# Optimization experiments

Hardware: AMD Instinct MI355X
Metric: run time of the kernel (lower is better)

## Reference

```python
import jax, jax.numpy as jnp
import numpy as np

N = 100000
E = 1600000
F_IN, H, C = 128, 128, 64


def setup_inputs() -> dict:
    key = jax.random.key(0)
    ks = jax.random.split(key, 8)
    x = jax.random.normal(ks[0], (N, F_IN), dtype=jnp.float32)
    edge_index = jax.random.randint(ks[1], (2, E), 0, N, dtype=jnp.int64)
    s = lambda fi: (1.0 / np.sqrt(fi))
    # SAGEConv1: lin_l (applied to mean-aggregated neighbors, has bias), lin_r (root, no bias)
    W1l = jax.random.uniform(ks[2], (H, F_IN), jnp.float32, -s(F_IN), s(F_IN))
    b1 = jnp.zeros((H,), jnp.float32)
    W1r = jax.random.uniform(ks[3], (H, F_IN), jnp.float32, -s(F_IN), s(F_IN))
    # SAGEConv2
    W2l = jax.random.uniform(ks[4], (C, H), jnp.float32, -s(H), s(H))
    b2 = jnp.zeros((C,), jnp.float32)
    W2r = jax.random.uniform(ks[5], (C, H), jnp.float32, -s(H), s(H))
    return {"x": x, "edge_index": edge_index, "W1l": W1l, "b1": b1, "W1r": W1r,
            "W2l": W2l, "b2": b2, "W2r": W2r}


def _mean_aggr(x, src, dst):
    # mean over incoming neighbors (PyG flow: edge_index[0]=source -> edge_index[1]=target)
    msg = x[src]                                            # [E, F] big gather
    summed = jax.ops.segment_sum(msg, dst, num_segments=N)  # [N, F]
    cnt = jax.ops.segment_sum(jnp.ones((src.shape[0],), x.dtype), dst, num_segments=N)
    return summed / jnp.clip(cnt, 1.0)[:, None]


def _sage_conv(x, src, dst, Wl, b, Wr):
    agg = _mean_aggr(x, src, dst)
    return agg @ Wl.T + b + x @ Wr.T


def _iconv(x, src, dst):
    # weight-free GCN propagation: D^-1/2 (A + I) D^-1/2 @ x
    loops = jnp.arange(N, dtype=src.dtype)
    s2 = jnp.concatenate([src, loops])
    d2 = jnp.concatenate([dst, loops])
    deg = jax.ops.segment_sum(jnp.ones((s2.shape[0],), x.dtype), d2, num_segments=N)
    dis = jnp.where(deg > 0, jax.lax.rsqrt(jnp.maximum(deg, 1.0)), 0.0)
    norm = dis[s2] * dis[d2]                               # [E+N]
    return jax.ops.segment_sum(norm[:, None] * x[s2], d2, num_segments=N)


def reference(x, edge_index, W1l, b1, W1r, W2l, b2, W2r):
    src, dst = edge_index[0], edge_index[1]
    h = jax.nn.relu(_sage_conv(x, src, dst, W1l, b1, W1r))
    # F.dropout(training=False) -> identity in eval mode
    h = _sage_conv(h, src, dst, W2l, b2, W2r)
    return _iconv(h, src, dst)
```

## Files before the change

kernel.cpp:

```cpp
#include <hip/hip_runtime.h>

#define GN 100000
#define GE 1600000
#define GF 128
#define GH 128
#define GC 64

#define NB 392
#define SLABSZ 5376
#define P1_EDGES 4096
#define P1_BLOCKS ((GE + P1_EDGES - 1) / P1_EDGES)
#define CASTX_BLOCKS 12500

typedef __attribute__((ext_vector_type(8))) short v8s;
typedef __attribute__((ext_vector_type(4))) float v4f;
typedef __attribute__((ext_vector_type(2))) float v2f;

__device__ __forceinline__ unsigned short f2bf(float f) {
    union { float f; unsigned u; } a; a.f = f;
    unsigned r = a.u + 0x7fff + ((a.u >> 16) & 1);
    return (unsigned short)(r >> 16);
}
__device__ __forceinline__ float bf2f(unsigned short b) {
    union { unsigned u; float f; } a; a.u = ((unsigned)b) << 16;
    return a.f;
}
__device__ __forceinline__ v2f cvt2(unsigned w) {
    union { unsigned u; float f; } lo, hi;
    lo.u = w << 16; hi.u = w & 0xffff0000u;
    return (v2f){lo.f, hi.f};
}

__device__ __forceinline__ int block_excl_scan256(int v, volatile int* ws, int tid) {
    int lane = tid & 63, w = tid >> 6;
    int s = v;
    #pragma unroll
    for (int off = 1; off < 64; off <<= 1) {
        int t = __shfl_up(s, off);
        if (lane >= off) s += t;
    }
    if (lane == 63) ws[w] = s;
    __syncthreads();
    int wbase = 0;
    if (w > 0) wbase += ws[0];
    if (w > 1) wbase += ws[1];
    if (w > 2) wbase += ws[2];
    __syncthreads();
    return wbase + s - v;
}

__global__ __launch_bounds__(256) void prep_kernel(
    unsigned* __restrict__ slab, int* __restrict__ bucket_cnt,
    const int* __restrict__ src, const int* __restrict__ dst,
    unsigned short* __restrict__ xb, const float* __restrict__ x,
    unsigned short* w1l, unsigned short* w1r,
    unsigned short* w2l, unsigned short* w2r,
    const float* W1l, const float* W1r,
    const float* W2l, const float* W2r)
{
    __shared__ int hist[512];
    __shared__ int scanex[512];
    __shared__ int cursor[512];
    __shared__ int gbase[512];
    __shared__ int wsS[4];
    __shared__ unsigned stage[P1_EDGES];
    __shared__ unsigned short sbid[P1_EDGES];

    int tid = threadIdx.x;
    int blk = blockIdx.x;

    if (blk >= P1_BLOCKS) {
        int cb = blk - P1_BLOCKS;
        if (cb < CASTX_BLOCKS) {
            int i = cb * 256 + tid;
            float4 v = ((const float4*)x)[i];
            ushort4 u;
            u.x = f2bf(v.x); u.y = f2bf(v.y); u.z = f2bf(v.z); u.w = f2bf(v.w);
            ((ushort4*)xb)[i] = u;
            return;
        }
        int i = (cb - CASTX_BLOCKS) * 256 + tid;
        const float* s; unsigned short* d; int off;
        if      (i <  4096) { s = W1l; d = w1l; off = i; }
        else if (i <  8192) { s = W1r; d = w1r; off = i - 4096; }
        else if (i < 10240) { s = W2l; d = w2l; off = i - 8192; }
        else if (i < 12288) { s = W2r; d = w2r; off = i - 10240; }
        else return;
        float4 v = ((const float4*)s)[off];
        ushort4 u;
        u.x = f2bf(v.x); u.y = f2bf(v.y); u.z = f2bf(v.z); u.w = f2bf(v.w);
        ((ushort4*)d)[off] = u;
        return;
    }

    int e0 = blk * P1_EDGES;
    int nE = min(P1_EDGES, GE - e0);

    unsigned pk[16]; int bk[16];
    hist[tid] = 0; hist[tid + 256] = 0;
    __syncthreads();
    #pragma unroll
    for (int j = 0; j < 16; ++j) {
        int i = j * 256 + tid;
        if (i < nE) {
            int e = e0 + i;
            int d = dst[e], s = src[e];
            int b = d >> 8;
            pk[j] = ((unsigned)(d & 255) << 17) | (unsigned)s;
            bk[j] = b;
            atomicAdd(&hist[b], 1);
        } else bk[j] = -1;
    }
    __syncthreads();
    int a0 = hist[2 * tid], a1 = hist[2 * tid + 1];
    int pbase = block_excl_scan256(a0 + a1, wsS, tid);
    scanex[2 * tid] = pbase;          cursor[2 * tid] = pbase;
    scanex[2 * tid + 1] = pbase + a0; cursor[2 * tid + 1] = pbase + a0;
    __syncthreads();
    #pragma unroll
    for (int j = 0; j < 16; ++j) {
        if (bk[j] >= 0) {
            int pos = atomicAdd(&cursor[bk[j]], 1);
            stage[pos] = pk[j];
            sbid[pos] = (unsigned short)bk[j];
        }
    }
    for (int b = tid; b < NB; b += 256) {
        int c = hist[b];
        gbase[b] = c ? atomicAdd(&bucket_cnt[b], c) : 0;
    }
    __syncthreads();
    for (int i = tid; i < nE; i += 256) {
        int b = sbid[i];
        int go = gbase[b] + (i - scanex[b]);
        if (go < SLABSZ)
            slab[(size_t)b * SLABSZ + go] = stage[i];
    }
}

__global__ __launch_bounds__(256) void bucket_pass2_kernel(
    int* __restrict__ csr, int* __restrict__ row_ptr,
    float* __restrict__ invc, float* __restrict__ dis,
    const unsigned* __restrict__ slab, const int* __restrict__ bucket_cnt)
{
    __shared__ int deg_l[256];
    __shared__ int cur[256];
    __shared__ int wsS[4];
    __shared__ int bstart_s;
    __shared__ unsigned stage[SLABSZ];

    int t = threadIdx.x;
    int b = blockIdx.x;

    int c0 = (2 * t < NB) ? bucket_cnt[2 * t] : 0;
    int c1 = (2 * t + 1 < NB) ? bucket_cnt[2 * t + 1] : 0;
    int pb = block_excl_scan256(c0 + c1, wsS, t);
    if (2 * t == b)     bstart_s = pb;
    if (2 * t + 1 == b) bstart_s = pb + c0;
    if (b == NB - 1 && t == 0) row_ptr[GN] = GE;

    int cnt = min(bucket_cnt[b], SLABSZ);
    const unsigned* sp = slab + (size_t)b * SLABSZ;
    deg_l[t] = 0;
    __syncthreads();
    int base = bstart_s;
    for (int i = t; i < cnt; i += 256)
        atomicAdd(&deg_l[sp[i] >> 17], 1);
    __syncthreads();
    int dg = deg_l[t];
    int ex = block_excl_scan256(dg, wsS, t);
    cur[t] = ex;
    __syncthreads();
    int d = b * 256 + t;
    if (d < GN) {
        row_ptr[d] = base + ex;
        float c = (float)dg;
        invc[d] = 1.0f / fmaxf(c, 1.0f);
        dis[d] = rsqrtf(c + 1.0f);
    }
    for (int i = t; i < cnt; i += 256) {
        unsigned p = sp[i];
        int pos = atomicAdd(&cur[p >> 17], 1);
        stage[pos] = p & 0x1FFFFu;
    }
    __syncthreads();
    for (int i = t; i < cnt; i += 256)
        csr[base + i] = (int)stage[i];
}

__global__ __launch_bounds__(64, 2) void fused_gemm_kernel(
    unsigned short* __restrict__ P, unsigned short* __restrict__ Q,
    const unsigned short* __restrict__ A1, const unsigned short* __restrict__ A2,
    const unsigned short* __restrict__ W1, const unsigned short* __restrict__ W2,
    const unsigned short* __restrict__ Wl, const unsigned short* __restrict__ Wr,
    const float* __restrict__ b1, const float* __restrict__ b2, int M)
{
    __shared__ unsigned short hs[64][136];

    int lane = threadIdx.x;
    int lm = lane & 15, quad = lane >> 4;
    int m_base = blockIdx.x * 64;

    v4f acc[4][8];
    #pragma unroll
    for (int mt = 0; mt < 4; ++mt)
        #pragma unroll
        for (int nt = 0; nt < 8; ++nt) acc[mt][nt] = (v4f){0.f,0.f,0.f,0.f};

    #pragma unroll
    for (int ks = 0; ks < 4; ++ks) {
        int koff = ks * 32 + quad * 8;
        v8s a1[4], a2[4];
        #pragma unroll
        for (int mt = 0; mt < 4; ++mt) {
            int row = m_base + mt * 16 + lm;
            if (row < M) {
                a1[mt] = *(const v8s*)(A1 + (size_t)row * 128 + koff);
                a2[mt] = *(const v8s*)(A2 + (size_t)row * 128 + koff);
            } else {
                a1[mt] = (v8s){0,0,0,0,0,0,0,0};
                a2[mt] = (v8s){0,0,0,0,0,0,0,0};
            }
        }
        v8s w1[8], w2[8];
        #pragma unroll
        for (int nt = 0; nt < 8; ++nt) {
            int col = nt * 16 + lm;
            w1[nt] = *(const v8s*)(W1 + (size_t)col * 128 + koff);
            w2[nt] = *(const v8s*)(W2 + (size_t)col * 128 + koff);
        }
        #pragma unroll
        for (int mt = 0; mt < 4; ++mt)
            #pragma unroll
            for (int nt = 0; nt < 8; ++nt) {
                acc[mt][nt] = __builtin_amdgcn_mfma_f32_16x16x32_bf16(a1[mt], w1[nt], acc[mt][nt], 0, 0, 0);
                acc[mt][nt] = __builtin_amdgcn_mfma_f32_16x16x32_bf16(a2[mt], w2[nt], acc[mt][nt], 0, 0, 0);
            }
    }

    #pragma unroll
    for (int mt = 0; mt < 4; ++mt)
        #pragma unroll
        for (int r = 0; r < 4; ++r) {
            int rl = mt * 16 + quad * 4 + r;
            #pragma unroll
            for (int nt = 0; nt < 8; ++nt) {
                int col = nt * 16 + lm;
                float v = acc[mt][nt][r] + b1[col];
                hs[rl][col] = f2bf(fmaxf(v, 0.f));
            }
        }

    v4f accP[4][4], accQ[4][4];
    #pragma unroll
    for (int mt = 0; mt < 4; ++mt)
        #pragma unroll
        for (int nt = 0; nt < 4; ++nt) {
            accP[mt][nt] = (v4f){0.f,0.f,0.f,0.f};
            accQ[mt][nt] = (v4f){0.f,0.f,0.f,0.f};
        }

    #pragma unroll
    for (int ks = 0; ks < 4; ++ks) {
        int koff = ks * 32 + quad * 8;
        v8s af[4], bl[4], br[4];
        #pragma unroll
        for (int mt = 0; mt < 4; ++mt)
            af[mt] = *(const v8s*)&hs[mt * 16 + lm][koff];
        #pragma unroll
        for (int nt = 0; nt < 4; ++nt) {
            int col = nt * 16 + lm;
            bl[nt] = *(const v8s*)(Wl + (size_t)col * 128 + koff);
            br[nt] = *(const v8s*)(Wr + (size_t)col * 128 + koff);
        }
        #pragma unroll
        for (int mt = 0; mt < 4; ++mt)
            #pragma unroll
            for (int nt = 0; nt < 4; ++nt) {
                accP[mt][nt] = __builtin_amdgcn_mfma_f32_16x16x32_bf16(af[mt], bl[nt], accP[mt][nt], 0, 0, 0);
                accQ[mt][nt] = __builtin_amdgcn_mfma_f32_16x16x32_bf16(af[mt], br[nt], accQ[mt][nt], 0, 0, 0);
            }
    }

    #pragma unroll
    for (int mt = 0; mt < 4; ++mt)
        #pragma unroll
        for (int r = 0; r < 4; ++r) {
            int row = m_base + mt * 16 + quad * 4 + r;
            if (row >= M) continue;
            #pragma unroll
            for (int nt = 0; nt < 4; ++nt) {
                int col = nt * 16 + lm;
                P[(size_t)row * 64 + col] = f2bf(accP[mt][nt][r]);
                Q[(size_t)row * 64 + col] = f2bf(accQ[mt][nt][r] + b2[col]);
            }
        }
}

__global__ __launch_bounds__(256) void gather_mean128_kernel(
    unsigned short* __restrict__ out, const unsigned short* __restrict__ in,
    const float* __restrict__ invc, const int* __restrict__ row_ptr,
    const int* __restrict__ csr, int N)
{
    int wid = (blockIdx.x * 256 + threadIdx.x) >> 6;
    int lane = threadIdx.x & 63;
    if (wid >= N) return;
    int beg = __builtin_amdgcn_readfirstlane(row_ptr[wid]);
    int end = __builtin_amdgcn_readfirstlane(row_ptr[wid + 1]);
    int d = end - beg;
    int grp = lane >> 4, lx = lane & 15;
    v2f a0 = {0.f,0.f}, a1 = {0.f,0.f}, a2 = {0.f,0.f}, a3 = {0.f,0.f};

    int nf = d >> 2;
    #pragma unroll 4
    for (int t = 0; t < nf; ++t) {
        int j = beg + t * 4;
        int s0 = csr[j], s1 = csr[j + 1], s2 = csr[j + 2], s3 = csr[j + 3];
        int sa = (lane & 16) ? s1 : s0;
        int sb = (lane & 16) ? s3 : s2;
        int ss = (lane & 32) ? sb : sa;
        uint4 v = ((const uint4*)(in + (size_t)ss * 128))[lx];
        a0 += cvt2(v.x); a1 += cvt2(v.y); a2 += cvt2(v.z); a3 += cvt2(v.w);
    }
    int rem = d & 3;
    if (rem) {
        int j = beg + nf * 4;
        int c1 = (rem > 1) ? 1 : 0;
        int c2 = (rem > 2) ? 2 : c1;
        int s0 = csr[j], s1 = csr[j + c1], s2 = csr[j + c2], s3 = s2;
        int sa = (lane & 16) ? s1 : s0;
        int sb = (lane & 16) ? s3 : s2;
        int ss = (lane & 32) ? sb : sa;
        uint4 v = ((const uint4*)(in + (size_t)ss * 128))[lx];
        bool ok = grp < rem;
        v.x = ok ? v.x : 0u; v.y = ok ? v.y : 0u;
        v.z = ok ? v.z : 0u; v.w = ok ? v.w : 0u;
        a0 += cvt2(v.x); a1 += cvt2(v.y); a2 += cvt2(v.z); a3 += cvt2(v.w);
    }
    a0.x += __shfl_xor(a0.x, 16); a0.y += __shfl_xor(a0.y, 16);
    a1.x += __shfl_xor(a1.x, 16); a1.y += __shfl_xor(a1.y, 16);
    a2.x += __shfl_xor(a2.x, 16); a2.y += __shfl_xor(a2.y, 16);
    a3.x += __shfl_xor(a3.x, 16); a3.y += __shfl_xor(a3.y, 16);
    a0.x += __shfl_xor(a0.x, 32); a0.y += __shfl_xor(a0.y, 32);
    a1.x += __shfl_xor(a1.x, 32); a1.y += __shfl_xor(a1.y, 32);
    a2.x += __shfl_xor(a2.x, 32); a2.y += __shfl_xor(a2.y, 32);
    a3.x += __shfl_xor(a3.x, 32); a3.y += __shfl_xor(a3.y, 32);
    if (grp == 0) {
        float ic = invc[wid];
        uint4 o;
        o.x = (unsigned)f2bf(a0.x * ic) | ((unsigned)f2bf(a0.y * ic) << 16);
        o.y = (unsigned)f2bf(a1.x * ic) | ((unsigned)f2bf(a1.y * ic) << 16);
        o.z = (unsigned)f2bf(a2.x * ic) | ((unsigned)f2bf(a2.y * ic) << 16);
        o.w = (unsigned)f2bf(a3.x * ic) | ((unsigned)f2bf(a3.y * ic) << 16);
        ((uint4*)(out + (size_t)wid * 128))[lx] = o;
    }
}

__global__ __launch_bounds__(256) void gather_combine_kernel(
    unsigned short* __restrict__ h2s, const unsigned short* __restrict__ p,
    const unsigned short* __restrict__ q,
    const float* __restrict__ invc, const float* __restrict__ dis,
    const int* __restrict__ row_ptr, const int* __restrict__ csr, int N)
{
    int wid = (blockIdx.x * 256 + threadIdx.x) >> 6;
    int lane = threadIdx.x & 63;
    if (wid >= N) return;
    int beg = __builtin_amdgcn_readfirstlane(row_ptr[wid]);
    int end = __builtin_amdgcn_readfirstlane(row_ptr[wid + 1]);
    int d = end - beg;
    int grp = lane >> 3, lx = lane & 7;
    v2f a0 = {0.f,0.f}, a1 = {0.f,0.f}, a2 = {0.f,0.f}, a3 = {0.f,0.f};

    int nf = d >> 3;
    #pragma unroll 2
    for (int t = 0; t < nf; ++t) {
        int j = beg + t * 8;
        int s0 = csr[j],     s1 = csr[j + 1], s2 = csr[j + 2], s3 = csr[j + 3];
        int s4 = csr[j + 4], s5 = csr[j + 5], s6 = csr[j + 6], s7 = csr[j + 7];
        int t0 = (lane & 8) ? s1 : s0; int t1 = (lane & 8) ? s3 : s2;
        int t2 = (lane & 8) ? s5 : s4; int t3 = (lane & 8) ? s7 : s6;
        int u0 = (lane & 16) ? t1 : t0; int u1 = (lane & 16) ? t3 : t2;
        int ss = (lane & 32) ? u1 : u0;
        uint4 v = ((const uint4*)(p + (size_t)ss * 64))[lx];
        a0 += cvt2(v.x); a1 += cvt2(v.y); a2 += cvt2(v.z); a3 += cvt2(v.w);
    }
    int rem = d & 7;
    if (rem) {
        int j = beg + nf * 8;
        int rc = rem - 1;
        int s0 = csr[j];
        int s1 = csr[j + min(1, rc)]; int s2 = csr[j + min(2, rc)];
        int s3 = csr[j + min(3, rc)]; int s4 = csr[j + min(4, rc)];
        int s5 = csr[j + min(5, rc)]; int s6 = csr[j + min(6, rc)];
        int s7 = csr[j + min(7, rc)];
        int t0 = (lane & 8) ? s1 : s0; int t1 = (lane & 8) ? s3 : s2;
        int t2 = (lane & 8) ? s5 : s4; int t3 = (lane & 8) ? s7 : s6;
        int u0 = (lane & 16) ? t1 : t0; int u1 = (lane & 16) ? t3 : t2;
        int ss = (lane & 32) ? u1 : u0;
        uint4 v = ((const uint4*)(p + (size_t)ss * 64))[lx];
        bool ok = grp < rem;
        v.x = ok ? v.x : 0u; v.y = ok ? v.y : 0u;
        v.z = ok ? v.z : 0u; v.w = ok ? v.w : 0u;
        a0 += cvt2(v.x); a1 += cvt2(v.y); a2 += cvt2(v.z); a3 += cvt2(v.w);
    }
    #pragma unroll
    for (int m = 8; m <= 32; m <<= 1) {
        a0.x += __shfl_xor(a0.x, m); a0.y += __shfl_xor(a0.y, m);
        a1.x += __shfl_xor(a1.x, m); a1.y += __shfl_xor(a1.y, m);
        a2.x += __shfl_xor(a2.x, m); a2.y += __shfl_xor(a2.y, m);
        a3.x += __shfl_xor(a3.x, m); a3.y += __shfl_xor(a3.y, m);
    }
    if (grp == 0) {
        float ic = invc[wid], dd = dis[wid];
        uint4 qv = ((const uint4*)(q + (size_t)wid * 64))[lx];
        v2f q0 = cvt2(qv.x), q1 = cvt2(qv.y), q2 = cvt2(qv.z), q3 = cvt2(qv.w);
        uint4 o;
        o.x = (unsigned)f2bf(dd * (a0.x * ic + q0.x)) | ((unsigned)f2bf(dd * (a0.y * ic + q0.y)) << 16);
        o.y = (unsigned)f2bf(dd * (a1.x * ic + q1.x)) | ((unsigned)f2bf(dd * (a1.y * ic + q1.y)) << 16);
        o.z = (unsigned)f2bf(dd * (a2.x * ic + q2.x)) | ((unsigned)f2bf(dd * (a2.y * ic + q2.y)) << 16);
        o.w = (unsigned)f2bf(dd * (a3.x * ic + q3.x)) | ((unsigned)f2bf(dd * (a3.y * ic + q3.y)) << 16);
        ((uint4*)(h2s + (size_t)wid * 64))[lx] = o;
    }
}

__global__ __launch_bounds__(256) void iconv_kernel(
    float* __restrict__ out, const unsigned short* __restrict__ h2s,
    const float* __restrict__ dis, const int* __restrict__ row_ptr,
    const int* __restrict__ csr, int N)
{
    int wid = (blockIdx.x * 256 + threadIdx.x) >> 6;
    int lane = threadIdx.x & 63;
    if (wid >= N) return;
    int beg = __builtin_amdgcn_readfirstlane(row_ptr[wid]);
    int end = __builtin_amdgcn_readfirstlane(row_ptr[wid + 1]);
    int d = end - beg;
    int grp = lane >> 3, lx = lane & 7;
    v2f a0 = {0.f,0.f}, a1 = {0.f,0.f}, a2 = {0.f,0.f}, a3 = {0.f,0.f};

    int nf = d >> 3;
    #pragma unroll 2
    for (int t = 0; t < nf; ++t) {
        int j = beg + t * 8;
        int s0 = csr[j],     s1 = csr[j + 1], s2 = csr[j + 2], s3 = csr[j + 3];
        int s4 = csr[j + 4], s5 = csr[j + 5], s6 = csr[j + 6], s7 = csr[j + 7];
        int t0 = (lane & 8) ? s1 : s0; int t1 = (lane & 8) ? s3 : s2;
        int t2 = (lane & 8) ? s5 : s4; int t3 = (lane & 8) ? s7 : s6;
        int u0 = (lane & 16) ? t1 : t0; int u1 = (lane & 16) ? t3 : t2;
        int ss = (lane & 32) ? u1 : u0;
        uint4 v = ((const uint4*)(h2s + (size_t)ss * 64))[lx];
        a0 += cvt2(v.x); a1 += cvt2(v.y); a2 += cvt2(v.z); a3 += cvt2(v.w);
    }
    int rem = d & 7;
    if (rem) {
        int j = beg + nf * 8;
        int rc = rem - 1;
        int s0 = csr[j];
        int s1 = csr[j + min(1, rc)]; int s2 = csr[j + min(2, rc)];
        int s3 = csr[j + min(3, rc)]; int s4 = csr[j + min(4, rc)];
        int s5 = csr[j + min(5, rc)]; int s6 = csr[j + min(6, rc)];
        int s7 = csr[j + min(7, rc)];
        int t0 = (lane & 8) ? s1 : s0; int t1 = (lane & 8) ? s3 : s2;
        int t2 = (lane & 8) ? s5 : s4; int t3 = (lane & 8) ? s7 : s6;
        int u0 = (lane & 16) ? t1 : t0; int u1 = (lane & 16) ? t3 : t2;
        int ss = (lane & 32) ? u1 : u0;
        uint4 v = ((const uint4*)(h2s + (size_t)ss * 64))[lx];
        bool ok = grp < rem;
        v.x = ok ? v.x : 0u; v.y = ok ? v.y : 0u;
        v.z = ok ? v.z : 0u; v.w = ok ? v.w : 0u;
        a0 += cvt2(v.x); a1 += cvt2(v.y); a2 += cvt2(v.z); a3 += cvt2(v.w);
    }
    #pragma unroll
    for (int m = 8; m <= 32; m <<= 1) {
        a0.x += __shfl_xor(a0.x, m); a0.y += __shfl_xor(a0.y, m);
        a1.x += __shfl_xor(a1.x, m); a1.y += __shfl_xor(a1.y, m);
        a2.x += __shfl_xor(a2.x, m); a2.y += __shfl_xor(a2.y, m);
        a3.x += __shfl_xor(a3.x, m); a3.y += __shfl_xor(a3.y, m);
    }
    if (grp == 0) {
        uint4 sv = ((const uint4*)(h2s + (size_t)wid * 64))[lx];
        v2f s0 = cvt2(sv.x), s1 = cvt2(sv.y), s2 = cvt2(sv.z), s3 = cvt2(sv.w);
        float dd = dis[wid];
        float4 o0 = make_float4(dd * (a0.x + s0.x), dd * (a0.y + s0.y),
                                dd * (a1.x + s1.x), dd * (a1.y + s1.y));
        float4 o1 = make_float4(dd * (a2.x + s2.x), dd * (a2.y + s2.y),
                                dd * (a3.x + s3.x), dd * (a3.y + s3.y));
        ((float4*)(out + (size_t)wid * 64))[lx * 2]     = o0;
        ((float4*)(out + (size_t)wid * 64))[lx * 2 + 1] = o1;
    }
}

extern "C" void kernel_launch(void* const* d_in, const int* in_sizes, int n_in,
                              void* d_out, int out_size, void* d_ws, size_t ws_size,
                              hipStream_t stream) {
    const float* x   = (const float*)d_in[0];
    const int*   ei  = (const int*)d_in[1];
    const float* W1l = (const float*)d_in[2];
    const float* b1  = (const float*)d_in[3];
    const float* W1r = (const float*)d_in[4];
    const float* W2l = (const float*)d_in[5];
    const float* b2  = (const float*)d_in[6];
    const float* W2r = (const float*)d_in[7];
    float* out = (float*)d_out;

    const int* src = ei;
    const int* dst = ei + GE;

    float* invc = (float*)d_ws;
    float* dis  = invc + GN;
    unsigned short* regA = (unsigned short*)(dis + GN);
    unsigned short* regB = regA + (size_t)GN * 128;
    unsigned short* xb    = regA;
    unsigned short* aggx  = regB;
    unsigned short* w1lb = regB + (size_t)GN * 128;
    unsigned short* w1rb = w1lb + GH * GF;
    unsigned short* w2lb = w1rb + GH * GF;
    unsigned short* w2rb = w2lb + GC * GH;
    int* row_ptr      = (int*)(w2rb + GC * GH);
    int* bucket_cnt   = row_ptr + GN + 1;
    unsigned* slab    = (unsigned*)(bucket_cnt + NB);
    int* csr          = (int*)(slab + (size_t)NB * SLABSZ);
    unsigned short* pq = (unsigned short*)(csr + GE);
    unsigned short* pb = pq;
    unsigned short* qb = pq + (size_t)GN * 64;
    unsigned short* h2s = regB;

    const int T = 256;
    const int g_wave = (GN * 64 + T - 1) / T;
    dim3 g_fused((GN + 63) / 64, 1);

    hipMemsetAsync(bucket_cnt, 0, NB * sizeof(int), stream);
    prep_kernel<<<P1_BLOCKS + CASTX_BLOCKS + 48, T, 0, stream>>>(
        slab, bucket_cnt, src, dst,
        xb, x, w1lb, w1rb, w2lb, w2rb, W1l, W1r, W2l, W2r);

    bucket_pass2_kernel<<<NB, T, 0, stream>>>(csr, row_ptr, invc, dis,
                                              slab, bucket_cnt);

    gather_mean128_kernel<<<g_wave, T, 0, stream>>>(aggx, xb, invc, row_ptr, csr, GN);

    fused_gemm_kernel<<<g_fused, 64, 0, stream>>>(pb, qb, aggx, xb,
                                                  w1lb, w1rb, w2lb, w2rb,
                                                  b1, b2, GN);

    gather_combine_kernel<<<g_wave, T, 0, stream>>>(h2s, pb, qb, invc, dis,
                                                    row_ptr, csr, GN);

    iconv_kernel<<<g_wave, T, 0, stream>>>(out, h2s, dis, row_ptr, csr, GN);
}
```

Measured before the change: 334.4 us.

## Halve GEMM tile height and split gather/GEMM launches into halves

Shrinks the fused GEMM block tile from 64 to 32 rows, loads weight fragments inside the MFMA loop instead of holding them all in registers, and raises the launch-bounds occupancy hint from 2 to 3. It also splits the gather and GEMM kernels into two launches covering half the rows each. The aim is to lower register pressure and raise occupancy in the GEMM. In exchange each weight fragment is reused across fewer rows, and the extra launches add overhead. The launches run back to back on one stream, so the split by itself gives no overlap.

```diff
diff --git a/kernel.cpp b/kernel.cpp
--- a/kernel.cpp
+++ b/kernel.cpp
@@ -188,31 +188,32 @@
         csr[base + i] = (int)stage[i];
 }
 
-__global__ __launch_bounds__(64, 2) void fused_gemm_kernel(
+__global__ __launch_bounds__(64, 3) void fused_gemm_kernel(
     unsigned short* __restrict__ P, unsigned short* __restrict__ Q,
     const unsigned short* __restrict__ A1, const unsigned short* __restrict__ A2,
     const unsigned short* __restrict__ W1, const unsigned short* __restrict__ W2,
     const unsigned short* __restrict__ Wl, const unsigned short* __restrict__ Wr,
-    const float* __restrict__ b1, const float* __restrict__ b2, int M)
+    const float* __restrict__ b1, const float* __restrict__ b2,
+    int m_off, int M)
 {
-    __shared__ unsigned short hs[64][136];
+    __shared__ unsigned short hs[32][136];
 
     int lane = threadIdx.x;
     int lm = lane & 15, quad = lane >> 4;
-    int m_base = blockIdx.x * 64;
-
-    v4f acc[4][8];
-    #pragma unroll
-    for (int mt = 0; mt < 4; ++mt)
+    int m_base = m_off + blockIdx.x * 32;
+
+    v4f acc[2][8];
+    #pragma unroll
+    for (int mt = 0; mt < 2; ++mt)
         #pragma unroll
         for (int nt = 0; nt < 8; ++nt) acc[mt][nt] = (v4f){0.f,0.f,0.f,0.f};
 
     #pragma unroll
     for (int ks = 0; ks < 4; ++ks) {
         int koff = ks * 32 + quad * 8;
-        v8s a1[4], a2[4];
-        #pragma unroll
-        for (int mt = 0; mt < 4; ++mt) {
+        v8s a1[2], a2[2];
+        #pragma unroll
+        for (int mt = 0; mt < 2; ++mt) {
             int row = m_base + mt * 16 + lm;
             if (row < M) {
                 a1[mt] = *(const v8s*)(A1 + (size_t)row * 128 + koff);
@@ -222,24 +223,21 @@
                 a2[mt] = (v8s){0,0,0,0,0,0,0,0};
             }
         }
-        v8s w1[8], w2[8];
         #pragma unroll
         for (int nt = 0; nt < 8; ++nt) {
             int col = nt * 16 + lm;
-            w1[nt] = *(const v8s*)(W1 + (size_t)col * 128 + koff);
-            w2[nt] = *(const v8s*)(W2 + (size_t)col * 128 + koff);
-        }
-        #pragma unroll
-        for (int mt = 0; mt < 4; ++mt)
+            v8s w1 = *(const v8s*)(W1 + (size_t)col * 128 + koff);
+            v8s w2 = *(const v8s*)(W2 + (size_t)col * 128 + koff);
             #pragma unroll
-            for (int nt = 0; nt < 8; ++nt) {
-                acc[mt][nt] = __builtin_amdgcn_mfma_f32_16x16x32_bf16(a1[mt], w1[nt], acc[mt][nt], 0, 0, 0);
-                acc[mt][nt] = __builtin_amdgcn_mfma_f32_16x16x32_bf16(a2[mt], w2[nt], acc[mt][nt], 0, 0, 0);
+            for (int mt = 0; mt < 2; ++mt) {
+                acc[mt][nt] = __builtin_amdgcn_mfma_f32_16x16x32_bf16(a1[mt], w1, acc[mt][nt], 0, 0, 0);
+                acc[mt][nt] = __builtin_amdgcn_mfma_f32_16x16x32_bf16(a2[mt], w2, acc[mt][nt], 0, 0, 0);
             }
-    }
-
-    #pragma unroll
-    for (int mt = 0; mt < 4; ++mt)
+        }
+    }
+
+    #pragma unroll
+    for (int mt = 0; mt < 2; ++mt)
         #pragma unroll
         for (int r = 0; r < 4; ++r) {
             int rl = mt * 16 + quad * 4 + r;
@@ -251,9 +249,9 @@
             }
         }
 
-    v4f accP[4][4], accQ[4][4];
-    #pragma unroll
-    for (int mt = 0; mt < 4; ++mt)
+    v4f accP[2][4], accQ[2][4];
+    #pragma unroll
+    for (int mt = 0; mt < 2; ++mt)
         #pragma unroll
         for (int nt = 0; nt < 4; ++nt) {
             accP[mt][nt] = (v4f){0.f,0.f,0.f,0.f};
@@ -263,27 +261,25 @@
     #pragma unroll
     for (int ks = 0; ks < 4; ++ks) {
         int koff = ks * 32 + quad * 8;
-        v8s af[4], bl[4], br[4];
-        #pragma unroll
-        for (int mt = 0; mt < 4; ++mt)
+        v8s af[2];
+        #pragma unroll
+        for (int mt = 0; mt < 2; ++mt)
             af[mt] = *(const v8s*)&hs[mt * 16 + lm][koff];
         #pragma unroll
         for (int nt = 0; nt < 4; ++nt) {
             int col = nt * 16 + lm;
-            bl[nt] = *(const v8s*)(Wl + (size_t)col * 128 + koff);
-            br[nt] = *(const v8s*)(Wr + (size_t)col * 128 + koff);
-        }
-        #pragma unroll
-        for (int mt = 0; mt < 4; ++mt)
+            v8s bl = *(const v8s*)(Wl + (size_t)col * 128 + koff);
+            v8s br = *(const v8s*)(Wr + (size_t)col * 128 + koff);
             #pragma unroll
-            for (int nt = 0; nt < 4; ++nt) {
-                accP[mt][nt] = __builtin_amdgcn_mfma_f32_16x16x32_bf16(af[mt], bl[nt], accP[mt][nt], 0, 0, 0);
-                accQ[mt][nt] = __builtin_amdgcn_mfma_f32_16x16x32_bf16(af[mt], br[nt], accQ[mt][nt], 0, 0, 0);
+            for (int mt = 0; mt < 2; ++mt) {
+                accP[mt][nt] = __builtin_amdgcn_mfma_f32_16x16x32_bf16(af[mt], bl, accP[mt][nt], 0, 0, 0);
+                accQ[mt][nt] = __builtin_amdgcn_mfma_f32_16x16x32_bf16(af[mt], br, accQ[mt][nt], 0, 0, 0);
             }
-    }
-
-    #pragma unroll
-    for (int mt = 0; mt < 4; ++mt)
+        }
+    }
+
+    #pragma unroll
+    for (int mt = 0; mt < 2; ++mt)
         #pragma unroll
         for (int r = 0; r < 4; ++r) {
             int row = m_base + mt * 16 + quad * 4 + r;
@@ -300,11 +296,11 @@
 __global__ __launch_bounds__(256) void gather_mean128_kernel(
     unsigned short* __restrict__ out, const unsigned short* __restrict__ in,
     const float* __restrict__ invc, const int* __restrict__ row_ptr,
-    const int* __restrict__ csr, int N)
+    const int* __restrict__ csr, int row0, int row1)
 {
-    int wid = (blockIdx.x * 256 + threadIdx.x) >> 6;
+    int wid = row0 + ((blockIdx.x * 256 + threadIdx.x) >> 6);
     int lane = threadIdx.x & 63;
-    if (wid >= N) return;
+    if (wid >= row1) return;
     int beg = __builtin_amdgcn_readfirstlane(row_ptr[wid]);
     int end = __builtin_amdgcn_readfirstlane(row_ptr[wid + 1]);
     int d = end - beg;
@@ -360,11 +356,12 @@
     unsigned short* __restrict__ h2s, const unsigned short* __restrict__ p,
     const unsigned short* __restrict__ q,
     const float* __restrict__ invc, const float* __restrict__ dis,
-    const int* __restrict__ row_ptr, const int* __restrict__ csr, int N)
+    const int* __restrict__ row_ptr, const int* __restrict__ csr,
+    int row0, int row1)
 {
-    int wid = (blockIdx.x * 256 + threadIdx.x) >> 6;
+    int wid = row0 + ((blockIdx.x * 256 + threadIdx.x) >> 6);
     int lane = threadIdx.x & 63;
-    if (wid >= N) return;
+    if (wid >= row1) return;
     int beg = __builtin_amdgcn_readfirstlane(row_ptr[wid]);
     int end = __builtin_amdgcn_readfirstlane(row_ptr[wid + 1]);
     int d = end - beg;
@@ -526,7 +523,7 @@
 
     const int T = 256;
     const int g_wave = (GN * 64 + T - 1) / T;
-    dim3 g_fused((GN + 63) / 64, 1);
+    const int g_half = (50000 * 64) / T;
 
     hipMemsetAsync(bucket_cnt, 0, NB * sizeof(int), stream);
     prep_kernel<<<P1_BLOCKS + CASTX_BLOCKS + 48, T, 0, stream>>>(
@@ -536,14 +533,22 @@
     bucket_pass2_kernel<<<NB, T, 0, stream>>>(csr, row_ptr, invc, dis,
                                               slab, bucket_cnt);
 
-    gather_mean128_kernel<<<g_wave, T, 0, stream>>>(aggx, xb, invc, row_ptr, csr, GN);
-
-    fused_gemm_kernel<<<g_fused, 64, 0, stream>>>(pb, qb, aggx, xb,
-                                                  w1lb, w1rb, w2lb, w2rb,
-                                                  b1, b2, GN);
-
-    gather_combine_kernel<<<g_wave, T, 0, stream>>>(h2s, pb, qb, invc, dis,
-                                                    row_ptr, csr, GN);
+    gather_mean128_kernel<<<g_half, T, 0, stream>>>(aggx, xb, invc, row_ptr, csr,
+                                                    0, 50000);
+    gather_mean128_kernel<<<g_half, T, 0, stream>>>(aggx, xb, invc, row_ptr, csr,
+                                                    50000, GN);
+
+    fused_gemm_kernel<<<1563, 64, 0, stream>>>(pb, qb, aggx, xb,
+                                               w1lb, w1rb, w2lb, w2rb,
+                                               b1, b2, 0, GN);
+    fused_gemm_kernel<<<1562, 64, 0, stream>>>(pb, qb, aggx, xb,
+                                               w1lb, w1rb, w2lb, w2rb,
+                                               b1, b2, 50016, GN);
+
+    gather_combine_kernel<<<g_half, T, 0, stream>>>(h2s, pb, qb, invc, dis,
+                                                    row_ptr, csr, 0, 50000);
+    gather_combine_kernel<<<g_half, T, 0, stream>>>(h2s, pb, qb, invc, dis,
+                                                    row_ptr, csr, 50000, GN);
 
     iconv_kernel<<<g_wave, T, 0, stream>>>(out, h2s, dis, row_ptr, csr, GN);
 }
```

Result: slower. 360.7 us (+7.9%).

## Fuse first-layer mean aggregation into the SAGE GEMM kernel via LDS

Applied to the files above, without the earlier changes.

Merges the 128-wide neighbor mean gather and the two-layer fused GEMM into one kernel. Each 1024-thread block handles 16 nodes: 16 waves each gather one node's neighbors into LDS, then 8 waves compute the first layer with MFMA, and finally the P/Q projections. This removes the aggx write and re-read through global memory and one kernel launch. In exchange the weight reuse per block drops from 64 to 16 rows, weights are reloaded much more often, and half the waves sit idle during the GEMM phases.

```diff
diff --git a/kernel.cpp b/kernel.cpp
--- a/kernel.cpp
+++ b/kernel.cpp
@@ -188,171 +188,118 @@
         csr[base + i] = (int)stage[i];
 }
 
-__global__ __launch_bounds__(64, 2) void fused_gemm_kernel(
+__global__ __launch_bounds__(1024, 8) void sage16_kernel(
     unsigned short* __restrict__ P, unsigned short* __restrict__ Q,
-    const unsigned short* __restrict__ A1, const unsigned short* __restrict__ A2,
+    const unsigned short* __restrict__ xb,
     const unsigned short* __restrict__ W1, const unsigned short* __restrict__ W2,
     const unsigned short* __restrict__ Wl, const unsigned short* __restrict__ Wr,
-    const float* __restrict__ b1, const float* __restrict__ b2, int M)
+    const float* __restrict__ b1, const float* __restrict__ b2,
+    const float* __restrict__ invc, const int* __restrict__ row_ptr,
+    const int* __restrict__ csr)
 {
-    __shared__ unsigned short hs[64][136];
-
-    int lane = threadIdx.x;
+    __shared__ unsigned short hsA[16][136];
+    __shared__ unsigned short hsB[16][136];
+
+    int tid = threadIdx.x;
+    int wv = tid >> 6, lane = tid & 63;
     int lm = lane & 15, quad = lane >> 4;
-    int m_base = blockIdx.x * 64;
-
-    v4f acc[4][8];
-    #pragma unroll
-    for (int mt = 0; mt < 4; ++mt)
+    int m_base = blockIdx.x * 16;
+
+    {
+        int wid = m_base + wv;
+        int beg = __builtin_amdgcn_readfirstlane(row_ptr[wid]);
+        int end = __builtin_amdgcn_readfirstlane(row_ptr[wid + 1]);
+        int d = end - beg;
+        v2f a0 = {0.f,0.f}, a1 = {0.f,0.f}, a2 = {0.f,0.f}, a3 = {0.f,0.f};
+
+        int nf = d >> 2;
+        #pragma unroll 4
+        for (int t = 0; t < nf; ++t) {
+            int j = beg + t * 4;
+            int s0 = csr[j], s1 = csr[j + 1], s2 = csr[j + 2], s3 = csr[j + 3];
+            int sa = (lane & 16) ? s1 : s0;
+            int sb = (lane & 16) ? s3 : s2;
+            int ss = (lane & 32) ? sb : sa;
+            uint4 v = ((const uint4*)(xb + (size_t)ss * 128))[lm];
+            a0 += cvt2(v.x); a1 += cvt2(v.y); a2 += cvt2(v.z); a3 += cvt2(v.w);
+        }
+        int rem = d & 3;
+        if (rem) {
+            int j = beg + nf * 4;
+            int c1 = (rem > 1) ? 1 : 0;
+            int c2 = (rem > 2) ? 2 : c1;
+            int s0 = csr[j], s1 = csr[j + c1], s2 = csr[j + c2], s3 = s2;
+            int sa = (lane & 16) ? s1 : s0;
+            int sb = (lane & 16) ? s3 : s2;
+            int ss = (lane & 32) ? sb : sa;
+            uint4 v = ((const uint4*)(xb + (size_t)ss * 128))[lm];
+            bool ok = quad < rem;
+            v.x = ok ? v.x : 0u; v.y = ok ? v.y : 0u;
+            v.z = ok ? v.z : 0u; v.w = ok ? v.w : 0u;
+            a0 += cvt2(v.x); a1 += cvt2(v.y); a2 += cvt2(v.z); a3 += cvt2(v.w);
+        }
+        a0.x += __shfl_xor(a0.x, 16); a0.y += __shfl_xor(a0.y, 16);
+        a1.x += __shfl_xor(a1.x, 16); a1.y += __shfl_xor(a1.y, 16);
+        a2.x += __shfl_xor(a2.x, 16); a2.y += __shfl_xor(a2.y, 16);
+        a3.x += __shfl_xor(a3.x, 16); a3.y += __shfl_xor(a3.y, 16);
+        a0.x += __shfl_xor(a0.x, 32); a0.y += __shfl_xor(a0.y, 32);
+        a1.x += __shfl_xor(a1.x, 32); a1.y += __shfl_xor(a1.y, 32);
+        a2.x += __shfl_xor(a2.x, 32); a2.y += __shfl_xor(a2.y, 32);
+        a3.x += __shfl_xor(a3.x, 32); a3.y += __shfl_xor(a3.y, 32);
+        if (quad == 0) {
+            float ic = invc[wid];
+            uint4 o;
+            o.x = (unsigned)f2bf(a0.x * ic) | ((unsigned)f2bf(a0.y * ic) << 16);
+            o.y = (unsigned)f2bf(a1.x * ic) | ((unsigned)f2bf(a1.y * ic) << 16);
+            o.z = (unsigned)f2bf(a2.x * ic) | ((unsigned)f2bf(a2.y * ic) << 16);
+            o.w = (unsigned)f2bf(a3.x * ic) | ((unsigned)f2bf(a3.y * ic) << 16);
+            *(uint4*)&hsA[wv][lm * 8] = o;
+        }
+    }
+    __syncthreads();
+
+    if (wv < 8) {
+        int col = wv * 16 + lm;
+        v4f acc = (v4f){0.f,0.f,0.f,0.f};
         #pragma unroll
-        for (int nt = 0; nt < 8; ++nt) acc[mt][nt] = (v4f){0.f,0.f,0.f,0.f};
-
-    #pragma unroll
-    for (int ks = 0; ks < 4; ++ks) {
-        int koff = ks * 32 + quad * 8;
-        v8s a1[4], a2[4];
+        for (int ks = 0; ks < 4; ++ks) {
+            int koff = ks * 32 + quad * 8;
+            v8s a1f = *(const v8s*)&hsA[lm][koff];
+            v8s w1 = *(const v8s*)(W1 + (size_t)col * 128 + koff);
+            acc = __builtin_amdgcn_mfma_f32_16x16x32_bf16(a1f, w1, acc, 0, 0, 0);
+            v8s a2f = *(const v8s*)(xb + (size_t)(m_base + lm) * 128 + koff);
+            v8s w2 = *(const v8s*)(W2 + (size_t)col * 128 + koff);
+            acc = __builtin_amdgcn_mfma_f32_16x16x32_bf16(a2f, w2, acc, 0, 0, 0);
+        }
+        float bv = b1[col];
         #pragma unroll
-        for (int mt = 0; mt < 4; ++mt) {
-            int row = m_base + mt * 16 + lm;
-            if (row < M) {
-                a1[mt] = *(const v8s*)(A1 + (size_t)row * 128 + koff);
-                a2[mt] = *(const v8s*)(A2 + (size_t)row * 128 + koff);
-            } else {
-                a1[mt] = (v8s){0,0,0,0,0,0,0,0};
-                a2[mt] = (v8s){0,0,0,0,0,0,0,0};
-            }
-        }
-        v8s w1[8], w2[8];
+        for (int r = 0; r < 4; ++r)
+            hsB[quad * 4 + r][col] = f2bf(fmaxf(acc[r] + bv, 0.f));
+    }
+    __syncthreads();
+
+    if (wv < 8) {
+        int isQ = wv >> 2;
+        int col = (wv & 3) * 16 + lm;
+        const unsigned short* W = isQ ? Wr : Wl;
+        v4f acc = (v4f){0.f,0.f,0.f,0.f};
         #pragma unroll
-        for (int nt = 0; nt < 8; ++nt) {
-            int col = nt * 16 + lm;
-            w1[nt] = *(const v8s*)(W1 + (size_t)col * 128 + koff);
-            w2[nt] = *(const v8s*)(W2 + (size_t)col * 128 + koff);
-        }
-        #pragma unroll
-        for (int mt = 0; mt < 4; ++mt)
+        for (int ks = 0; ks < 4; ++ks) {
+            int koff = ks * 32 + quad * 8;
+            v8s af = *(const v8s*)&hsB[lm][koff];
+            v8s bw = *(const v8s*)(W + (size_t)col * 128 + koff);
+            acc = __builtin_amdgcn_mfma_f32_16x16x32_bf16(af, bw, acc, 0, 0, 0);
+        }
+        if (isQ) {
+            float bv = b2[col];
             #pragma unroll
-            for (int nt = 0; nt < 8; ++nt) {
-                acc[mt][nt] = __builtin_amdgcn_mfma_f32_16x16x32_bf16(a1[mt], w1[nt], acc[mt][nt], 0, 0, 0);
-                acc[mt][nt] = __builtin_amdgcn_mfma_f32_16x16x32_bf16(a2[mt], w2[nt], acc[mt][nt], 0, 0, 0);
-            }
-    }
-
-    #pragma unroll
-    for (int mt = 0; mt < 4; ++mt)
-        #pragma unroll
-        for (int r = 0; r < 4; ++r) {
-            int rl = mt * 16 + quad * 4 + r;
+            for (int r = 0; r < 4; ++r)
+                Q[(size_t)(m_base + quad * 4 + r) * 64 + col] = f2bf(acc[r] + bv);
+        } else {
             #pragma unroll
-            for (int nt = 0; nt < 8; ++nt) {
-                int col = nt * 16 + lm;
-                float v = acc[mt][nt][r] + b1[col];
-                hs[rl][col] = f2bf(fmaxf(v, 0.f));
-            }
-        }
-
-    v4f accP[4][4], accQ[4][4];
-    #pragma unroll
-    for (int mt = 0; mt < 4; ++mt)
-        #pragma unroll
-        for (int nt = 0; nt < 4; ++nt) {
-            accP[mt][nt] = (v4f){0.f,0.f,0.f,0.f};
-            accQ[mt][nt] = (v4f){0.f,0.f,0.f,0.f};
-        }
-
-    #pragma unroll
-    for (int ks = 0; ks < 4; ++ks) {
-        int koff = ks * 32 + quad * 8;
-        v8s af[4], bl[4], br[4];
-        #pragma unroll
-        for (int mt = 0; mt < 4; ++mt)
-            af[mt] = *(const v8s*)&hs[mt * 16 + lm][koff];
-        #pragma unroll
-        for (int nt = 0; nt < 4; ++nt) {
-            int col = nt * 16 + lm;
-            bl[nt] = *(const v8s*)(Wl + (size_t)col * 128 + koff);
-            br[nt] = *(const v8s*)(Wr + (size_t)col * 128 + koff);
-        }
-        #pragma unroll
-        for (int mt = 0; mt < 4; ++mt)
-            #pragma unroll
-            for (int nt = 0; nt < 4; ++nt) {
-                accP[mt][nt] = __builtin_amdgcn_mfma_f32_16x16x32_bf16(af[mt], bl[nt], accP[mt][nt], 0, 0, 0);
-                accQ[mt][nt] = __builtin_amdgcn_mfma_f32_16x16x32_bf16(af[mt], br[nt], accQ[mt][nt], 0, 0, 0);
-            }
-    }
-
-    #pragma unroll
-    for (int mt = 0; mt < 4; ++mt)
-        #pragma unroll
-        for (int r = 0; r < 4; ++r) {
-            int row = m_base + mt * 16 + quad * 4 + r;
-            if (row >= M) continue;
-            #pragma unroll
-            for (int nt = 0; nt < 4; ++nt) {
-                int col = nt * 16 + lm;
-                P[(size_t)row * 64 + col] = f2bf(accP[mt][nt][r]);
-                Q[(size_t)row * 64 + col] = f2bf(accQ[mt][nt][r] + b2[col]);
-            }
-        }
-}
-
-__global__ __launch_bounds__(256) void gather_mean128_kernel(
-    unsigned short* __restrict__ out, const unsigned short* __restrict__ in,
-    const float* __restrict__ invc, const int* __restrict__ row_ptr,
-    const int* __restrict__ csr, int N)
-{
-    int wid = (blockIdx.x * 256 + threadIdx.x) >> 6;
-    int lane = threadIdx.x & 63;
-    if (wid >= N) return;
-    int beg = __builtin_amdgcn_readfirstlane(row_ptr[wid]);
-    int end = __builtin_amdgcn_readfirstlane(row_ptr[wid + 1]);
-    int d = end - beg;
-    int grp = lane >> 4, lx = lane & 15;
-    v2f a0 = {0.f,0.f}, a1 = {0.f,0.f}, a2 = {0.f,0.f}, a3 = {0.f,0.f};
-
-    int nf = d >> 2;
-    #pragma unroll 4
-    for (int t = 0; t < nf; ++t) {
-        int j = beg + t * 4;
-        int s0 = csr[j], s1 = csr[j + 1], s2 = csr[j + 2], s3 = csr[j + 3];
-        int sa = (lane & 16) ? s1 : s0;
-        int sb = (lane & 16) ? s3 : s2;
-        int ss = (lane & 32) ? sb : sa;
-        uint4 v = ((const uint4*)(in + (size_t)ss * 128))[lx];
-        a0 += cvt2(v.x); a1 += cvt2(v.y); a2 += cvt2(v.z); a3 += cvt2(v.w);
-    }
-    int rem = d & 3;
-    if (rem) {
-        int j = beg + nf * 4;
-        int c1 = (rem > 1) ? 1 : 0;
-        int c2 = (rem > 2) ? 2 : c1;
-        int s0 = csr[j], s1 = csr[j + c1], s2 = csr[j + c2], s3 = s2;
-        int sa = (lane & 16) ? s1 : s0;
-        int sb = (lane & 16) ? s3 : s2;
-        int ss = (lane & 32) ? sb : sa;
-        uint4 v = ((const uint4*)(in + (size_t)ss * 128))[lx];
-        bool ok = grp < rem;
-        v.x = ok ? v.x : 0u; v.y = ok ? v.y : 0u;
-        v.z = ok ? v.z : 0u; v.w = ok ? v.w : 0u;
-        a0 += cvt2(v.x); a1 += cvt2(v.y); a2 += cvt2(v.z); a3 += cvt2(v.w);
-    }
-    a0.x += __shfl_xor(a0.x, 16); a0.y += __shfl_xor(a0.y, 16);
-    a1.x += __shfl_xor(a1.x, 16); a1.y += __shfl_xor(a1.y, 16);
-    a2.x += __shfl_xor(a2.x, 16); a2.y += __shfl_xor(a2.y, 16);
-    a3.x += __shfl_xor(a3.x, 16); a3.y += __shfl_xor(a3.y, 16);
-    a0.x += __shfl_xor(a0.x, 32); a0.y += __shfl_xor(a0.y, 32);
-    a1.x += __shfl_xor(a1.x, 32); a1.y += __shfl_xor(a1.y, 32);
-    a2.x += __shfl_xor(a2.x, 32); a2.y += __shfl_xor(a2.y, 32);
-    a3.x += __shfl_xor(a3.x, 32); a3.y += __shfl_xor(a3.y, 32);
-    if (grp == 0) {
-        float ic = invc[wid];
-        uint4 o;
-        o.x = (unsigned)f2bf(a0.x * ic) | ((unsigned)f2bf(a0.y * ic) << 16);
-        o.y = (unsigned)f2bf(a1.x * ic) | ((unsigned)f2bf(a1.y * ic) << 16);
-        o.z = (unsigned)f2bf(a2.x * ic) | ((unsigned)f2bf(a2.y * ic) << 16);
-        o.w = (unsigned)f2bf(a3.x * ic) | ((unsigned)f2bf(a3.y * ic) << 16);
-        ((uint4*)(out + (size_t)wid * 128))[lx] = o;
+            for (int r = 0; r < 4; ++r)
+                P[(size_t)(m_base + quad * 4 + r) * 64 + col] = f2bf(acc[r]);
+        }
     }
 }
 
@@ -510,7 +457,6 @@
     unsigned short* regA = (unsigned short*)(dis + GN);
     unsigned short* regB = regA + (size_t)GN * 128;
     unsigned short* xb    = regA;
-    unsigned short* aggx  = regB;
     unsigned short* w1lb = regB + (size_t)GN * 128;
     unsigned short* w1rb = w1lb + GH * GF;
     unsigned short* w2lb = w1rb + GH * GF;
@@ -526,7 +472,6 @@
 
     const int T = 256;
     const int g_wave = (GN * 64 + T - 1) / T;
-    dim3 g_fused((GN + 63) / 64, 1);
 
     hipMemsetAsync(bucket_cnt, 0, NB * sizeof(int), stream);
     prep_kernel<<<P1_BLOCKS + CASTX_BLOCKS + 48, T, 0, stream>>>(
@@ -536,11 +481,9 @@
     bucket_pass2_kernel<<<NB, T, 0, stream>>>(csr, row_ptr, invc, dis,
                                               slab, bucket_cnt);
 
-    gather_mean128_kernel<<<g_wave, T, 0, stream>>>(aggx, xb, invc, row_ptr, csr, GN);
-
-    fused_gemm_kernel<<<g_fused, 64, 0, stream>>>(pb, qb, aggx, xb,
-                                                  w1lb, w1rb, w2lb, w2rb,
-                                                  b1, b2, GN);
+    sage16_kernel<<<GN / 16, 1024, 0, stream>>>(pb, qb, xb,
+                                                w1lb, w1rb, w2lb, w2rb,
+                                                b1, b2, invc, row_ptr, csr);
 
     gather_combine_kernel<<<g_wave, T, 0, stream>>>(h2s, pb, qb, invc, dis,
                                                     row_ptr, csr, GN);
```

Result: slower. 378.2 us (+13.1%).
